# Kernel optimization log

Hardware: AMD Instinct MI355X
Metric: run time of the kernel (lower is better)

Reference implementation:

```python
import jax, jax.numpy as jnp
import numpy as np

N, E, F, C = 100000, 1600000, 64, 256


def setup_inputs() -> dict:
    key = jax.random.key(0)
    ks = jax.random.split(key, 9)

    def lin(k, fi, fo):
        kw, kb = jax.random.split(k)
        w = jax.random.normal(kw, (fi, fo), jnp.float32) * np.float32(1.0 / np.sqrt(fi))
        b = jax.random.normal(kb, (fo,), jnp.float32) * 0.001
        return w, b

    content = jax.random.normal(ks[0], (N, C), jnp.float32)
    node_emb = jax.random.normal(ks[1], (N + 1, F), jnp.float32) * np.float32(1.0 / (100 * F))
    proj_w, proj_b = lin(ks[2], C, F)
    c0w1, c0b1 = lin(ks[3], 2 * F, 4 * F)   # first layer: inp=2F -> 4F
    c0w2, c0b2 = lin(ks[4], 4 * F, F)
    c1w1, c1b1 = lin(ks[5], 3 * F, 6 * F)   # prediction layer: inp=3F -> 6F
    c1w2, c1b2 = lin(ks[6], 6 * F, F)
    nid = jnp.arange(N, dtype=jnp.int32)
    src = jax.random.randint(ks[7], (E,), 0, N, dtype=jnp.int32)
    dst = jax.random.randint(ks[8], (E,), 0, N, dtype=jnp.int32)
    return dict(content=content, node_emb=node_emb, proj_w=proj_w, proj_b=proj_b,
                c0w1=c0w1, c0b1=c0b1, c0w2=c0w2, c0b2=c0b2,
                c1w1=c1w1, c1b1=c1b1, c1w2=c1w2, c1b2=c1b2,
                nid=nid, src=src, dst=dst)


def _l2norm(x):
    # per-node L2 renorm with clamp(min=1e-6) like torch .norm().clamp
    n = jnp.linalg.norm(x, axis=1, keepdims=True)
    return x / jnp.maximum(n, 1e-6)


def _forward(content, node_emb, proj_w, proj_b,
             c0w1, c0b1, c0w2, c0b2, c1w1, c1b1, c1w2, c1b2,
             nid, src, dst):
    n = content.shape[0]
    lrelu = lambda x: jax.nn.leaky_relu(x, 0.1)
    # node init: embedding + projected content (GaussianNoise is identity in eval)
    h = node_emb[nid + 1] + lrelu(content @ proj_w + proj_b)
    # w = sum of 'one' over in-neighbors = in-degree
    deg = jax.ops.segment_sum(jnp.ones(src.shape[0], h.dtype), dst, num_segments=n)
    wden = jnp.maximum(deg - 1.0, 1.0)[:, None]  # (w - 1).clamp(min=1)

    # ---- layer 0 (first_layer) ----
    h_agg = jax.ops.segment_sum(h[src], dst, num_segments=n)  # copy_src('h') + sum
    h_agg = (h_agg - h) / wden
    z = lrelu(jnp.concatenate([h, h_agg], axis=1) @ c0w1 + c0b1)
    h_new = _l2norm(lrelu(z @ c0w2 + c0b2))
    h_res = _l2norm(h_agg)  # skip is None since in_dims == out_dims
    h = h_new

    # ---- layer 1 (prediction_layer) ----
    h_agg = jax.ops.segment_sum(h[src], dst, num_segments=n)
    h_res_sum = jax.ops.segment_sum(h_res[src], dst, num_segments=n)
    h_agg = (h_agg - h) / wden
    z = lrelu(jnp.concatenate([h, h_agg, h_res_sum], axis=1) @ c1w1 + c1b1)
    h_new = z @ c1w2 + c1b2  # prediction layer: no trailing LeakyReLU
    return _l2norm(h_new)


def reference(content, node_emb, proj_w, proj_b, c0w1, c0b1, c0w2, c0b2,
              c1w1, c1b1, c1w2, c1b2, nid, src, dst):
    return _forward(content, node_emb, proj_w, proj_b,
                    c0w1, c0b1, c0w2, c0b2, c1w1, c1b1, c1w2, c1b2,
                    nid, src, dst)
```

## Files before the change

kernel.cpp:

```cpp
#include <hip/hip_runtime.h>

typedef _Float16 half_t;
typedef half_t h8 __attribute__((ext_vector_type(8)));
typedef float f32x4 __attribute__((ext_vector_type(4)));
typedef unsigned int uint;
typedef unsigned long long ull;

__device__ __forceinline__ float lrelu_f(float x){ return x >= 0.f ? x : 0.1f*x; }

__device__ __forceinline__ float2 unpack_h2(uint v){
  half_t lo = __builtin_bit_cast(half_t, (unsigned short)(v & 0xffffu));
  half_t hi = __builtin_bit_cast(half_t, (unsigned short)(v >> 16));
  return make_float2((float)lo, (float)hi);
}
__device__ __forceinline__ uint pack_h2(float a, float b){
  unsigned short lo = __builtin_bit_cast(unsigned short, (half_t)a);
  unsigned short hi = __builtin_bit_cast(unsigned short, (half_t)b);
  return (uint)lo | ((uint)hi << 16);
}

enum { EPI_INIT=0, EPI_LRELU=1, EPI_LRELU_L2=2, EPI_L2=3 };
constexpr int CAP = 64;
constexpr int SLOT = 768;

__global__ void pack_all_kernel(const float* __restrict__ s0, half_t* __restrict__ d0,
                                const float* __restrict__ s1, half_t* __restrict__ d1,
                                const float* __restrict__ s2, half_t* __restrict__ d2,
                                const float* __restrict__ s3, half_t* __restrict__ d3,
                                const float* __restrict__ s4, half_t* __restrict__ d4){
  int b = blockIdx.x;
  const float* w; half_t* o; int K, M;
  if      (b < 8)  { w=s0; o=d0; K=256; M=64;  }
  else if (b < 24) { w=s1; o=d1; K=128; M=256; b-=8; }
  else if (b < 32) { w=s2; o=d2; K=256; M=64;  b-=24; }
  else if (b < 68) { w=s3; o=d3; K=192; M=384; b-=32; }
  else             { w=s4; o=d4; K=384; M=64;  b-=68; }
  int idx = b*256 + threadIdx.x;
  int total = (K/32)*(M/16)*64;
  if (idx >= total) return;
  int lane = idx & 63;
  int t = idx >> 6;
  int CBn = M/16;
  int cb = t % CBn;
  int s  = t / CBn;
  int k0 = s*32 + (lane>>4)*8;
  int c  = cb*16 + (lane&15);
  #pragma unroll
  for (int j=0;j<8;++j) o[(size_t)idx*8 + j] = (half_t)w[(size_t)(k0+j)*M + c];
}

template<int IT>
__global__ __launch_bounds__(256) void binA_kernel(const int* __restrict__ src, const int* __restrict__ dst,
    ull* __restrict__ staging, int* __restrict__ cntsPC, int E, int n){
  __shared__ int lcnt[8];
  if (threadIdx.x < 8) lcnt[threadIdx.x] = 0;
  __syncthreads();
  int chunk = blockIdx.x;
  long base = (long)chunk * (256*IT);
  #pragma unroll
  for (int it=0; it<IT; ++it){
    long i = base + it*256 + threadIdx.x;
    if (i < E){
      int d = __builtin_nontemporal_load(dst + i);
      int s = __builtin_nontemporal_load(src + i);
      int p = (int)(((long)d*8)/n);
      int pos = atomicAdd(&lcnt[p], 1);
      if (pos < SLOT)
        staging[((size_t)chunk*8 + p)*SLOT + pos] = ((ull)(uint)d << 32) | (uint)s;
    }
  }
  __syncthreads();
  if (threadIdx.x < 8){
    int c = lcnt[threadIdx.x];
    cntsPC[chunk*8 + threadIdx.x] = c < SLOT ? c : SLOT;
  }
}

__global__ __launch_bounds__(256) void scatB_kernel(const ull* __restrict__ staging,
    const int* __restrict__ cntsPC, int* __restrict__ cnt, int* __restrict__ col){
  int b = blockIdx.x;
  int c = cntsPC[b];
  const ull* sp = staging + (size_t)b*SLOT;
  for (int j = threadIdx.x; j < c; j += 256){
    ull v = __builtin_nontemporal_load(sp + j);
    int d = (int)(v >> 32);
    int s = (int)(v & 0xffffffffu);
    int r = atomicAdd(&cnt[d], 1);
    if (r < CAP) col[(size_t)d*CAP + r] = s;
  }
}

template<int K, int MOUT, int EPI>
__global__ __launch_bounds__(256) void gemm_kernel(
  const float* __restrict__ x0, int st0,
  const half_t* __restrict__ wp, const float* __restrict__ bias,
  half_t* __restrict__ outv, int ost,
  const float* __restrict__ emb, const int* __restrict__ nid, int n)
{
  constexpr int KS = K/32;
  constexpr int CB = MOUT/16;
  const int lane = threadIdx.x & 63;
  const int wid  = threadIdx.x >> 6;
  const int row0 = blockIdx.x*64 + wid*16;
  const int arow = row0 + (lane & 15);
  const int arowc = arow < n ? arow : n-1;
  const int khi = (lane>>4)*8;

  f32x4 acc[CB];
  #pragma unroll
  for (int cb=0;cb<CB;++cb) acc[cb] = (f32x4){0.f,0.f,0.f,0.f};

  #pragma unroll
  for (int s=0;s<KS;++s){
    int k0 = s*32 + khi;
    f32x4 a0 = *(const f32x4*)(x0 + (size_t)arowc*st0 + k0);
    f32x4 a1 = *(const f32x4*)(x0 + (size_t)arowc*st0 + k0 + 4);
    h8 af;
    #pragma unroll
    for (int j=0;j<4;++j){ af[j]=(half_t)a0[j]; af[j+4]=(half_t)a1[j]; }
    const h8* wrow = (const h8*)wp + (size_t)(s*CB)*64 + lane;
    #pragma unroll
    for (int cb=0;cb<CB;++cb){
      h8 bf = wrow[cb*64];
      acc[cb] = __builtin_amdgcn_mfma_f32_16x16x32_f16(af, bf, acc[cb], 0,0,0);
    }
  }

  const int cgrp = lane >> 4;
  const int ccol = lane & 15;
  #pragma unroll
  for (int r=0;r<4;++r){
    int R = row0 + cgrp*4 + r;
    if (R < n){
      #pragma unroll
      for (int cb=0;cb<CB;++cb){
        float t = lrelu_f(acc[cb][r] + bias[cb*16+ccol]);
        if constexpr (EPI==EPI_INIT) t += emb[(size_t)(nid[R]+1)*64 + cb*16 + ccol];
        outv[(size_t)R*ost + cb*16 + ccol] = (half_t)t;
      }
    }
  }
}

template<int K1, int M1, int M2, int NSRC, int EPI2, bool OUTF16>
__global__ __launch_bounds__(256,4) void mlp_kernel(
  const half_t* __restrict__ x0, const half_t* __restrict__ x1, const half_t* __restrict__ x2,
  int st0, int st1, int st2,
  const half_t* __restrict__ wp1, const float* __restrict__ b1,
  const half_t* __restrict__ wp2, const float* __restrict__ b2,
  void* __restrict__ outv, int ost, int n)
{
  constexpr int RS  = 17;
  constexpr int KS1 = K1/32, CBT = M1/16, CBW = CBT/4;
  constexpr int KS2 = M1/32, CB2 = M2/16;
  constexpr int RED = 65;
  __shared__ uint  zc[M1*RS];
  __shared__ float red[2*16*RED];

  const int lane = threadIdx.x & 63;
  const int wid  = threadIdx.x >> 6;
  const int row0 = blockIdx.x*32;
  const int khi  = (lane>>4)*8;
  const int ccol = lane & 15;
  const int cgrp = lane >> 4;

  f32x4 acc[2][CBW];
  #pragma unroll
  for (int t=0;t<2;++t)
    #pragma unroll
    for (int cb=0;cb<CBW;++cb) acc[t][cb] = (f32x4){0.f,0.f,0.f,0.f};

  #pragma unroll
  for (int s=0;s<KS1;++s){
    int k0 = s*32 + khi;
    const half_t* p = x0; int st = st0; int koff = k0;
    if constexpr (NSRC>1){
      int isrc = k0 >> 6;
      if constexpr (NSRC>=2){ if (isrc==1){ p=x1; st=st1; } }
      if constexpr (NSRC>=3){ if (isrc==2){ p=x2; st=st2; } }
      koff = k0 & 63;
    }
    h8 af[2];
    #pragma unroll
    for (int t=0;t<2;++t){
      int ar = row0 + t*16 + ccol; if (ar >= n) ar = n-1;
      af[t] = *(const h8*)(p + (size_t)ar*st + koff);
    }
    #pragma unroll
    for (int cb=0;cb<CBW;++cb){
      h8 bf = ((const h8*)wp1)[(size_t)(s*CBT + wid*CBW + cb)*64 + lane];
      #pragma unroll
      for (int t=0;t<2;++t)
        acc[t][cb] = __builtin_amdgcn_mfma_f32_16x16x32_f16(af[t], bf, acc[t][cb], 0,0,0);
    }
  }
  #pragma unroll
  for (int t=0;t<2;++t){
    #pragma unroll
    for (int cb=0;cb<CBW;++cb){
      int col = wid*(CBW*16) + cb*16 + ccol;
      float bb = b1[col];
      float v0 = lrelu_f(acc[t][cb][0]+bb);
      float v1 = lrelu_f(acc[t][cb][1]+bb);
      float v2 = lrelu_f(acc[t][cb][2]+bb);
      float v3 = lrelu_f(acc[t][cb][3]+bb);
      int idx = col*RS + t*8 + cgrp*2;
      zc[idx]   = pack_h2(v0,v1);
      zc[idx+1] = pack_h2(v2,v3);
    }
  }
  __syncthreads();

  const int rt = wid & 1, kh = wid >> 1;
  f32x4 acc2[CB2];
  #pragma unroll
  for (int cb=0;cb<CB2;++cb) acc2[cb] = (f32x4){0.f,0.f,0.f,0.f};
  const uint sel = (lane&1) ? 0x07060302u : 0x05040100u;
  const int rp0 = rt*8 + (ccol>>1);

  #pragma unroll
  for (int si=0;si<KS2/2;++si){
    int s = kh*(KS2/2) + si;
    uint v[8];
    #pragma unroll
    for (int j=0;j<8;++j) v[j] = zc[(s*32 + khi + j)*RS + rp0];
    uint4 u;
    u.x = __builtin_amdgcn_perm(v[1], v[0], sel);
    u.y = __builtin_amdgcn_perm(v[3], v[2], sel);
    u.z = __builtin_amdgcn_perm(v[5], v[4], sel);
    u.w = __builtin_amdgcn_perm(v[7], v[6], sel);
    h8 af2 = __builtin_bit_cast(h8, u);
    #pragma unroll
    for (int cb=0;cb<CB2;++cb){
      h8 bf = ((const h8*)wp2)[(size_t)(s*CB2+cb)*64 + lane];
      acc2[cb] = __builtin_amdgcn_mfma_f32_16x16x32_f16(af2, bf, acc2[cb], 0,0,0);
    }
  }
  if (kh == 1){
    #pragma unroll
    for (int cb=0;cb<CB2;++cb)
      #pragma unroll
      for (int r=0;r<4;++r)
        red[(rt*16 + cgrp*4 + r)*RED + cb*16 + ccol] = acc2[cb][r];
  }
  __syncthreads();
  if (kh == 0){
    #pragma unroll
    for (int r=0;r<4;++r){
      int Rr = row0 + rt*16 + cgrp*4 + r;
      float vv[CB2];
      #pragma unroll
      for (int cb=0;cb<CB2;++cb){
        float t = acc2[cb][r] + red[(rt*16 + cgrp*4 + r)*RED + cb*16 + ccol] + b2[cb*16+ccol];
        if constexpr (EPI2==EPI_LRELU_L2) t = lrelu_f(t);
        vv[cb] = t;
      }
      float sq = 0.f;
      #pragma unroll
      for (int cb=0;cb<CB2;++cb) sq += vv[cb]*vv[cb];
      sq += __shfl_xor(sq,1); sq += __shfl_xor(sq,2);
      sq += __shfl_xor(sq,4); sq += __shfl_xor(sq,8);
      float inv = 1.f / fmaxf(sqrtf(sq), 1e-6f);
      if (Rr < n){
        #pragma unroll
        for (int cb=0;cb<CB2;++cb){
          float t = vv[cb]*inv;
          if constexpr (OUTF16)
            ((half_t*)outv)[(size_t)Rr*ost + cb*16 + ccol] = (half_t)t;
          else
            ((float*)outv)[(size_t)Rr*ost + cb*16 + ccol] = t;
        }
      }
    }
  }
}

__global__ __launch_bounds__(256) void segsum0_kernel(const uint* __restrict__ hu, const int* __restrict__ cnt,
                               const int* __restrict__ col,
                               uint* __restrict__ hagg, uint* __restrict__ hc, int n){
  int node = blockIdx.x*4 + (threadIdx.x>>6);
  if (node >= n) return;
  int lane = threadIdx.x & 63;
  int g = lane >> 3, l = lane & 7;
  int deg = cnt[node];
  int degc = deg < CAP ? deg : CAP;
  const int* cv = col + (size_t)node*CAP;
  float a[8] = {0,0,0,0,0,0,0,0};
  int j = g;
  for (; j + 8 < degc; j += 16){
    int c0 = cv[j], c1 = cv[j+8];
    uint4 v0 = *(const uint4*)(hu + (size_t)c0*32 + l*4);
    uint4 v1 = *(const uint4*)(hu + (size_t)c1*32 + l*4);
    float2 f0=unpack_h2(v0.x), f1=unpack_h2(v0.y), f2=unpack_h2(v0.z), f3=unpack_h2(v0.w);
    float2 g0=unpack_h2(v1.x), g1=unpack_h2(v1.y), g2=unpack_h2(v1.z), g3=unpack_h2(v1.w);
    a[0]+=f0.x+g0.x; a[1]+=f0.y+g0.y; a[2]+=f1.x+g1.x; a[3]+=f1.y+g1.y;
    a[4]+=f2.x+g2.x; a[5]+=f2.y+g2.y; a[6]+=f3.x+g3.x; a[7]+=f3.y+g3.y;
  }
  if (j < degc){
    int c = cv[j];
    uint4 v = *(const uint4*)(hu + (size_t)c*32 + l*4);
    float2 f0=unpack_h2(v.x), f1=unpack_h2(v.y), f2=unpack_h2(v.z), f3=unpack_h2(v.w);
    a[0]+=f0.x; a[1]+=f0.y; a[2]+=f1.x; a[3]+=f1.y;
    a[4]+=f2.x; a[5]+=f2.y; a[6]+=f3.x; a[7]+=f3.y;
  }
  #pragma unroll
  for (int q=0;q<8;++q){
    a[q] += __shfl_xor(a[q], 8);
    a[q] += __shfl_xor(a[q], 16);
    a[q] += __shfl_xor(a[q], 32);
  }
  uint4 hv4 = *(const uint4*)(hu + (size_t)node*32 + l*4);
  float2 b0=unpack_h2(hv4.x), b1=unpack_h2(hv4.y), b2=unpack_h2(hv4.z), b3=unpack_h2(hv4.w);
  float hv[8] = {b0.x,b0.y,b1.x,b1.y,b2.x,b2.y,b3.x,b3.y};
  float iwd = 1.f / fmaxf((float)deg - 1.f, 1.f);
  float sq = 0.f;
  #pragma unroll
  for (int q=0;q<8;++q){ a[q] = (a[q]-hv[q])*iwd; sq += a[q]*a[q]; }
  sq += __shfl_xor(sq,1); sq += __shfl_xor(sq,2); sq += __shfl_xor(sq,4);
  float inv = 1.f / fmaxf(sqrtf(sq), 1e-6f);
  if (g == 0){
    uint4 oa, oh;
    oa.x = pack_h2(a[0],a[1]); oa.y = pack_h2(a[2],a[3]);
    oa.z = pack_h2(a[4],a[5]); oa.w = pack_h2(a[6],a[7]);
    oh.x = pack_h2(a[0]*inv,a[1]*inv); oh.y = pack_h2(a[2]*inv,a[3]*inv);
    oh.z = pack_h2(a[4]*inv,a[5]*inv); oh.w = pack_h2(a[6]*inv,a[7]*inv);
    *(uint4*)(hagg + (size_t)node*32 + l*4) = oa;
    *(uint4*)(hc + (size_t)node*64 + 32 + l*4) = oh;
  }
}

__global__ __launch_bounds__(256) void segsum1_kernel(const uint* __restrict__ hcu, const int* __restrict__ cnt,
                               const int* __restrict__ col,
                               uint* __restrict__ hagg, uint* __restrict__ hsum, int n){
  int node = blockIdx.x*4 + (threadIdx.x>>6);
  if (node >= n) return;
  int lane = threadIdx.x & 63;
  int g = lane >> 4, l = lane & 15;
  int deg = cnt[node];
  int degc = deg < CAP ? deg : CAP;
  const int* cv = col + (size_t)node*CAP;
  float a[8] = {0,0,0,0,0,0,0,0};
  int j = g;
  for (; j + 12 < degc; j += 16){
    int c0 = cv[j], c1 = cv[j+4], c2 = cv[j+8], c3 = cv[j+12];
    uint4 v0 = *(const uint4*)(hcu + (size_t)c0*64 + l*4);
    uint4 v1 = *(const uint4*)(hcu + (size_t)c1*64 + l*4);
    uint4 v2 = *(const uint4*)(hcu + (size_t)c2*64 + l*4);
    uint4 v3 = *(const uint4*)(hcu + (size_t)c3*64 + l*4);
    float2 e0, e1, e2, e3;
    e0=unpack_h2(v0.x); e1=unpack_h2(v0.y); e2=unpack_h2(v0.z); e3=unpack_h2(v0.w);
    a[0]+=e0.x; a[1]+=e0.y; a[2]+=e1.x; a[3]+=e1.y; a[4]+=e2.x; a[5]+=e2.y; a[6]+=e3.x; a[7]+=e3.y;
    e0=unpack_h2(v1.x); e1=unpack_h2(v1.y); e2=unpack_h2(v1.z); e3=unpack_h2(v1.w);
    a[0]+=e0.x; a[1]+=e0.y; a[2]+=e1.x; a[3]+=e1.y; a[4]+=e2.x; a[5]+=e2.y; a[6]+=e3.x; a[7]+=e3.y;
    e0=unpack_h2(v2.x); e1=unpack_h2(v2.y); e2=unpack_h2(v2.z); e3=unpack_h2(v2.w);
    a[0]+=e0.x; a[1]+=e0.y; a[2]+=e1.x; a[3]+=e1.y; a[4]+=e2.x; a[5]+=e2.y; a[6]+=e3.x; a[7]+=e3.y;
    e0=unpack_h2(v3.x); e1=unpack_h2(v3.y); e2=unpack_h2(v3.z); e3=unpack_h2(v3.w);
    a[0]+=e0.x; a[1]+=e0.y; a[2]+=e1.x; a[3]+=e1.y; a[4]+=e2.x; a[5]+=e2.y; a[6]+=e3.x; a[7]+=e3.y;
  }
  for (; j < degc; j += 4){
    int c = cv[j];
    uint4 v = *(const uint4*)(hcu + (size_t)c*64 + l*4);
    float2 f0=unpack_h2(v.x), f1=unpack_h2(v.y), f2=unpack_h2(v.z), f3=unpack_h2(v.w);
    a[0]+=f0.x; a[1]+=f0.y; a[2]+=f1.x; a[3]+=f1.y;
    a[4]+=f2.x; a[5]+=f2.y; a[6]+=f3.x; a[7]+=f3.y;
  }
  #pragma unroll
  for (int q=0;q<8;++q){
    a[q] += __shfl_xor(a[q], 16);
    a[q] += __shfl_xor(a[q], 32);
  }
  if (g == 0){
    if (l < 8){
      uint4 hv4 = *(const uint4*)(hcu + (size_t)node*64 + l*4);
      float2 b0=unpack_h2(hv4.x), b1=unpack_h2(hv4.y), b2=unpack_h2(hv4.z), b3=unpack_h2(hv4.w);
      float hv[8] = {b0.x,b0.y,b1.x,b1.y,b2.x,b2.y,b3.x,b3.y};
      float iwd = 1.f / fmaxf((float)deg - 1.f, 1.f);
      uint4 o;
      o.x = pack_h2((a[0]-hv[0])*iwd,(a[1]-hv[1])*iwd);
      o.y = pack_h2((a[2]-hv[2])*iwd,(a[3]-hv[3])*iwd);
      o.z = pack_h2((a[4]-hv[4])*iwd,(a[5]-hv[5])*iwd);
      o.w = pack_h2((a[6]-hv[6])*iwd,(a[7]-hv[7])*iwd);
      *(uint4*)(hagg + (size_t)node*32 + l*4) = o;
    } else {
      uint4 o;
      o.x = pack_h2(a[0],a[1]); o.y = pack_h2(a[2],a[3]);
      o.z = pack_h2(a[4],a[5]); o.w = pack_h2(a[6],a[7]);
      *(uint4*)(hsum + (size_t)node*32 + (l-8)*4) = o;
    }
  }
}

extern "C" void kernel_launch(void* const* d_in, const int* in_sizes, int n_in,
                              void* d_out, int out_size, void* d_ws, size_t ws_size,
                              hipStream_t stream){
  const float* content = (const float*)d_in[0];
  const float* node_emb= (const float*)d_in[1];
  const float* proj_w  = (const float*)d_in[2];
  const float* proj_b  = (const float*)d_in[3];
  const float* c0w1 = (const float*)d_in[4];
  const float* c0b1 = (const float*)d_in[5];
  const float* c0w2 = (const float*)d_in[6];
  const float* c0b2 = (const float*)d_in[7];
  const float* c1w1 = (const float*)d_in[8];
  const float* c1b1 = (const float*)d_in[9];
  const float* c1w2 = (const float*)d_in[10];
  const float* c1b2 = (const float*)d_in[11];
  const int* nid = (const int*)d_in[12];
  const int* src = (const int*)d_in[13];
  const int* dst = (const int*)d_in[14];
  float* out = (float*)d_out;
  const int n = in_sizes[12];
  const int E = in_sizes[13];

  char* ws = (char*)d_ws;
  size_t off = 0;
  auto alloc = [&](size_t bytes)->char*{
    char* p = ws + off;
    off = (off + bytes + 255) & ~(size_t)255;
    return p;
  };
  const int nChunks = (E + 2047)/2048;
  half_t* h0   = (half_t*)alloc((size_t)n*64*2);
  half_t* hc   = (half_t*)alloc((size_t)n*128*2);
  half_t* hagg0= (half_t*)alloc((size_t)n*64*2);
  half_t* hagg1= (half_t*)alloc((size_t)n*64*2);
  half_t* hsum1= (half_t*)alloc((size_t)n*64*2);
  int* cnt    = (int*)alloc((size_t)n*4);
  int* col    = (int*)alloc((size_t)n*CAP*4);
  ull* staging= (ull*)alloc((size_t)nChunks*8*SLOT*8);
  int* cntsPC = (int*)alloc((size_t)nChunks*8*4);
  half_t* wp0 = (half_t*)alloc((size_t)256*64*2);
  half_t* wp1 = (half_t*)alloc((size_t)128*256*2);
  half_t* wp2 = (half_t*)alloc((size_t)256*64*2);
  half_t* wp3 = (half_t*)alloc((size_t)192*384*2);
  half_t* wp4 = (half_t*)alloc((size_t)384*64*2);

  hipMemsetAsync(cnt, 0, (size_t)n*4, stream);

  pack_all_kernel<<<80,256,0,stream>>>(proj_w, wp0, c0w1, wp1, c0w2, wp2, c1w1, wp3, c1w2, wp4);

  binA_kernel<8><<<nChunks,256,0,stream>>>(src, dst, staging, cntsPC, E, n);
  scatB_kernel<<<nChunks*8,256,0,stream>>>(staging, cntsPC, cnt, col);

  const int rgrid = (n + 63)/64;
  const int mgrid = (n + 31)/32;

  gemm_kernel<256,64,EPI_INIT><<<rgrid,256,0,stream>>>(
      content, 256, wp0, proj_b, h0, 64, node_emb, nid, n);

  segsum0_kernel<<<(n+3)/4,256,0,stream>>>((const uint*)h0, cnt, col,
                                           (uint*)hagg0, (uint*)hc, n);
  mlp_kernel<128,256,64,2,EPI_LRELU_L2,true><<<mgrid,256,0,stream>>>(
      h0, hagg0, nullptr, 64,64,0, wp1, c0b1, wp2, c0b2, hc, 128, n);

  segsum1_kernel<<<(n+3)/4,256,0,stream>>>((const uint*)hc, cnt, col,
                                           (uint*)hagg1, (uint*)hsum1, n);
  mlp_kernel<192,384,64,3,EPI_L2,false><<<mgrid,256,0,stream>>>(
      hc, hagg1, hsum1, 128,64,64, wp3, c1b1, wp4, c1b2, out, 64, n);
}
```

Before: 301.7 us.

## Replace 8-way edge binning with 128-node bucket sort and LDS-counted scatter

```diff
diff --git a/kernel.cpp b/kernel.cpp
--- a/kernel.cpp
+++ b/kernel.cpp
@@ -5,6 +5,7 @@
 typedef float f32x4 __attribute__((ext_vector_type(4)));
 typedef unsigned int uint;
 typedef unsigned long long ull;
+typedef unsigned short ushort;
 
 __device__ __forceinline__ float lrelu_f(float x){ return x >= 0.f ? x : 0.1f*x; }
 
@@ -21,7 +22,8 @@
 
 enum { EPI_INIT=0, EPI_LRELU=1, EPI_LRELU_L2=2, EPI_L2=3 };
 constexpr int CAP = 64;
-constexpr int SLOT = 768;
+constexpr int CHUNK = 4096;
+constexpr int OSTR = 1056;
 
 __global__ void pack_all_kernel(const float* __restrict__ s0, half_t* __restrict__ d0,
                                 const float* __restrict__ s1, half_t* __restrict__ d1,
@@ -49,44 +51,74 @@
   for (int j=0;j<8;++j) o[(size_t)idx*8 + j] = (half_t)w[(size_t)(k0+j)*M + c];
 }
 
-template<int IT>
 __global__ __launch_bounds__(256) void binA_kernel(const int* __restrict__ src, const int* __restrict__ dst,
-    ull* __restrict__ staging, int* __restrict__ cntsPC, int E, int n){
-  __shared__ int lcnt[8];
-  if (threadIdx.x < 8) lcnt[threadIdx.x] = 0;
-  __syncthreads();
-  int chunk = blockIdx.x;
-  long base = (long)chunk * (256*IT);
-  #pragma unroll
-  for (int it=0; it<IT; ++it){
-    long i = base + it*256 + threadIdx.x;
+    ull* __restrict__ staging, ushort* __restrict__ offs, int E, int nb){
+  __shared__ int hist[1024];
+  __shared__ int cursor[1024];
+  int c = blockIdx.x;
+  int base = c * CHUNK;
+  for (int j = threadIdx.x; j < 1024; j += 256) hist[j] = 0;
+  __syncthreads();
+  #pragma unroll
+  for (int it=0; it<CHUNK/256; ++it){
+    int i = base + it*256 + threadIdx.x;
+    if (i < E) atomicAdd(&hist[dst[i] >> 7], 1);
+  }
+  __syncthreads();
+  for (int off=1; off<1024; off<<=1){
+    int v[4];
+    #pragma unroll
+    for (int k=0;k<4;++k){
+      int j = threadIdx.x + k*256;
+      v[k] = (j>=off)? hist[j-off] : 0;
+    }
+    __syncthreads();
+    #pragma unroll
+    for (int k=0;k<4;++k) hist[threadIdx.x + k*256] += v[k];
+    __syncthreads();
+  }
+  for (int j = threadIdx.x; j < 1024; j += 256){
+    int ex = j ? hist[j-1] : 0;
+    cursor[j] = ex;
+    if (j <= nb) offs[(size_t)c*OSTR + j] = (ushort)ex;
+  }
+  __syncthreads();
+  #pragma unroll
+  for (int it=0; it<CHUNK/256; ++it){
+    int i = base + it*256 + threadIdx.x;
     if (i < E){
-      int d = __builtin_nontemporal_load(dst + i);
-      int s = __builtin_nontemporal_load(src + i);
-      int p = (int)(((long)d*8)/n);
-      int pos = atomicAdd(&lcnt[p], 1);
-      if (pos < SLOT)
-        staging[((size_t)chunk*8 + p)*SLOT + pos] = ((ull)(uint)d << 32) | (uint)s;
-    }
-  }
-  __syncthreads();
-  if (threadIdx.x < 8){
-    int c = lcnt[threadIdx.x];
-    cntsPC[chunk*8 + threadIdx.x] = c < SLOT ? c : SLOT;
+      int d = dst[i];
+      int s = src[i];
+      int pos = atomicAdd(&cursor[d >> 7], 1);
+      staging[(size_t)c*CHUNK + pos] = ((ull)(uint)d << 32) | (uint)s;
+    }
   }
 }
 
 __global__ __launch_bounds__(256) void scatB_kernel(const ull* __restrict__ staging,
-    const int* __restrict__ cntsPC, int* __restrict__ cnt, int* __restrict__ col){
+    const ushort* __restrict__ offs, int* __restrict__ cnt, int* __restrict__ col,
+    int nChunks, int n){
+  __shared__ int lcnt[128];
   int b = blockIdx.x;
-  int c = cntsPC[b];
-  const ull* sp = staging + (size_t)b*SLOT;
-  for (int j = threadIdx.x; j < c; j += 256){
-    ull v = __builtin_nontemporal_load(sp + j);
-    int d = (int)(v >> 32);
-    int s = (int)(v & 0xffffffffu);
-    int r = atomicAdd(&cnt[d], 1);
-    if (r < CAP) col[(size_t)d*CAP + r] = s;
+  int node0 = b << 7;
+  if (threadIdx.x < 128) lcnt[threadIdx.x] = 0;
+  __syncthreads();
+  for (int c = threadIdx.x; c < nChunks; c += 256){
+    const ushort* op = offs + (size_t)c*OSTR;
+    int o0 = op[b], o1 = op[b+1];
+    const ull* sp = staging + (size_t)c*CHUNK;
+    for (int j = o0; j < o1; ++j){
+      ull v = sp[j];
+      int d = (int)(v >> 32);
+      int s = (int)(uint)v;
+      int r = atomicAdd(&lcnt[d & 127], 1);
+      if (r < CAP) col[(size_t)d*CAP + r] = s;
+    }
+  }
+  __syncthreads();
+  if (threadIdx.x < 128){
+    int node = node0 + threadIdx.x;
+    if (node < n) cnt[node] = lcnt[threadIdx.x];
   }
 }
 
@@ -419,7 +451,8 @@
     off = (off + bytes + 255) & ~(size_t)255;
     return p;
   };
-  const int nChunks = (E + 2047)/2048;
+  const int nChunks = (E + CHUNK - 1)/CHUNK;
+  const int nb = (n + 127) >> 7;
   half_t* h0   = (half_t*)alloc((size_t)n*64*2);
   half_t* hc   = (half_t*)alloc((size_t)n*128*2);
   half_t* hagg0= (half_t*)alloc((size_t)n*64*2);
@@ -427,20 +460,18 @@
   half_t* hsum1= (half_t*)alloc((size_t)n*64*2);
   int* cnt    = (int*)alloc((size_t)n*4);
   int* col    = (int*)alloc((size_t)n*CAP*4);
-  ull* staging= (ull*)alloc((size_t)nChunks*8*SLOT*8);
-  int* cntsPC = (int*)alloc((size_t)nChunks*8*4);
+  ull* staging= (ull*)alloc((size_t)nChunks*CHUNK*8);
+  ushort* offs= (ushort*)alloc((size_t)nChunks*OSTR*2);
   half_t* wp0 = (half_t*)alloc((size_t)256*64*2);
   half_t* wp1 = (half_t*)alloc((size_t)128*256*2);
   half_t* wp2 = (half_t*)alloc((size_t)256*64*2);
   half_t* wp3 = (half_t*)alloc((size_t)192*384*2);
   half_t* wp4 = (half_t*)alloc((size_t)384*64*2);
 
-  hipMemsetAsync(cnt, 0, (size_t)n*4, stream);
-
   pack_all_kernel<<<80,256,0,stream>>>(proj_w, wp0, c0w1, wp1, c0w2, wp2, c1w1, wp3, c1w2, wp4);
 
-  binA_kernel<8><<<nChunks,256,0,stream>>>(src, dst, staging, cntsPC, E, n);
-  scatB_kernel<<<nChunks*8,256,0,stream>>>(staging, cntsPC, cnt, col);
+  binA_kernel<<<nChunks,256,0,stream>>>(src, dst, staging, offs, E, nb);
+  scatB_kernel<<<nb,256,0,stream>>>(staging, offs, cnt, col, nChunks, n);
 
   const int rgrid = (n + 63)/64;
   const int mgrid = (n + 31)/32;
```

Result: faster. 279.5 us (-7.4%).
